# Optimization experiments

Measured on AMD Instinct MI355X. Metric: run time of the kernel, lower is better.

Reference implementation:

```python
import jax, jax.numpy as jnp
import numpy as np

N_RNA, N_PROT = 50000, 20000
S, E = 4, 500000
D_IN = 1024


def setup_inputs() -> dict:
    key = jax.random.key(0)
    ks = jax.random.split(key, 12)
    return {
        "rna_rows": jax.random.randint(ks[0], (S, E), 0, N_RNA, dtype=jnp.int32),
        "rna_cols": jax.random.randint(ks[1], (S, E), 0, N_PROT, dtype=jnp.int32),
        "rna_vals": jax.random.uniform(ks[2], (S, E), dtype=jnp.float32),
        "prot_rows": jax.random.randint(ks[3], (S, E), 0, N_PROT, dtype=jnp.int32),
        "prot_cols": jax.random.randint(ks[4], (S, E), 0, N_RNA, dtype=jnp.int32),
        "prot_vals": jax.random.uniform(ks[5], (S, E), dtype=jnp.float32),
        "H_rna": jax.random.normal(ks[6], (N_RNA, D_IN), dtype=jnp.float32),
        "H_prot": jax.random.normal(ks[7], (N_PROT, D_IN), dtype=jnp.float32),
        "w0": jax.random.normal(ks[8], (S, 1024, 128), dtype=jnp.float32) * 0.04,
        "sw0": jax.random.normal(ks[9], (1024, 512), dtype=jnp.float32) * 0.04,
        "w1": jax.random.normal(ks[10], (S, 512, 64), dtype=jnp.float32) * 0.06,
        "sw1": jax.random.normal(ks[11], (512, 256), dtype=jnp.float32) * 0.06,
    }


def _spmm_all(rows, cols, vals, x, n_out):
    # rows/cols/vals: [S, E]; x: [S, n_in, k] -> [S, n_out, k]
    def one(r, c, v, xs):
        return jax.ops.segment_sum(v[:, None] * xs[c], r, num_segments=n_out)
    return jax.vmap(one)(rows, cols, vals, x)


def reference(rna_rows, rna_cols, rna_vals, prot_rows, prot_cols, prot_vals,
              H_rna, H_prot, w0, sw0, w1, sw1):
    n_rna, n_prot = H_rna.shape[0], H_prot.shape[0]
    for W, SW in ((w0, sw0), (w1, sw1)):
        s, _, k = W.shape
        # per-relation dense transform: [S, n, k]
        tmp_u = jnp.einsum('nd,sdk->snk', H_rna, W)
        tmp_v = jnp.einsum('nd,sdk->snk', H_prot, W)
        # sparse aggregation across the bipartite graph
        rna_h = _spmm_all(rna_rows, rna_cols, rna_vals, tmp_v, n_rna)     # [S, n_rna, k]
        prot_h = _spmm_all(prot_rows, prot_cols, prot_vals, tmp_u, n_prot)
        # concat over relations (matches torch.cat along dim=1)
        rna_h = jnp.transpose(rna_h, (1, 0, 2)).reshape(n_rna, s * k)
        prot_h = jnp.transpose(prot_h, (1, 0, 2)).reshape(n_prot, s * k)
        # self-loop residual; dropout=0.0 (eval) is identity; relu activation
        H_rna = jax.nn.relu(rna_h + H_rna @ SW)
        H_prot = jax.nn.relu(prot_h + H_prot @ SW)
    return H_rna, H_prot
```

## Files before the change

kernel.cpp:

```cpp
#include <hip/hip_runtime.h>
#include <hip/hip_bf16.h>


typedef unsigned short u16;
typedef short s16x8 __attribute__((ext_vector_type(8)));
typedef float f32x4 __attribute__((ext_vector_type(4)));
typedef __attribute__((ext_vector_type(8))) unsigned short u16x8;
typedef __attribute__((ext_vector_type(2))) unsigned short u16x2;
typedef unsigned long long u64;

__device__ __forceinline__ u16 f2bf(float x) {
    unsigned u = __float_as_uint(x);
    return (u16)((u + 0x7fff + ((u >> 16) & 1)) >> 16);
}
__device__ __forceinline__ float bf2f(u16 h) {
    return __uint_as_float(((unsigned)h) << 16);
}

__device__ __forceinline__ void gload16(const u16* g, u16* l) {
    __builtin_amdgcn_global_load_lds(
        (const __attribute__((address_space(1))) unsigned int*)g,
        (__attribute__((address_space(3))) unsigned int*)l,
        16, 0, 0);
}

__global__ __launch_bounds__(256)
void gemm_bf16_kernel(const u16* __restrict__ Ah, const u16* __restrict__ Bh,
                      u16* __restrict__ Y, int ldy,
                      int K, int nxmask, int nxshift)
{
    __shared__ u16 lds[2][2][4096];

    const int nwg = gridDim.x;
    const int q   = nwg >> 3, r8 = nwg & 7;
    const int xcd = blockIdx.x & 7, pos = blockIdx.x >> 3;
    const int lin = (xcd < r8 ? xcd * (q + 1) : r8 * (q + 1) + (xcd - r8) * q) + pos;
    const int bm0 = (lin >> nxshift) * 128;
    const int bn0 = (lin & nxmask) * 128;

    const int tid  = threadIdx.x;
    const int lane = tid & 63;
    const int wid  = tid >> 6;
    const int wr   = wid >> 1;
    const int wc   = wid & 1;

    const int srow = tid >> 2;
    const int scol = ((tid & 3) ^ ((tid >> 3) & 3)) * 8;
    const size_t aoff0 = (size_t)(bm0 + srow) * K + scol;
    const size_t aoff1 = (size_t)(bm0 + srow + 64) * K + scol;
    const size_t boff0 = (size_t)(bn0 + srow) * K + scol;
    const size_t boff1 = (size_t)(bn0 + srow + 64) * K + scol;
    const int c0 = tid * 8;
    const int c1 = 2048 + tid * 8;

    u16* L0 = &lds[0][0][0];

    f32x4 zero = {0.f, 0.f, 0.f, 0.f};
    f32x4 acc[4][4];
    #pragma unroll
    for (int i = 0; i < 4; ++i)
        #pragma unroll
        for (int j = 0; j < 4; ++j) acc[i][j] = zero;

    const int fchunk = (((lane >> 4) ^ ((lane >> 1) & 3))) * 8;
    const int a_fr = (wr * 64 + (lane & 15)) * 32 + fchunk;
    const int b_fr = (wc * 64 + (lane & 15)) * 32 + fchunk;

    const int nk = K >> 5;

    {
        u16* L = L0;
        gload16(Ah + aoff0, L + c0);          gload16(Ah + aoff1, L + c1);
        gload16(Bh + boff0, L + 4096 + c0);   gload16(Bh + boff1, L + 4096 + c1);
    }
    int cur = 0;
    for (int t = 0; t < nk; ++t) {
        if (t + 1 < nk) {
            const int k0 = (t + 1) * 32;
            u16* L = L0 + (cur ^ 1) * 8192;
            gload16(Ah + aoff0 + k0, L + c0);         gload16(Ah + aoff1 + k0, L + c1);
            gload16(Bh + boff0 + k0, L + 4096 + c0);  gload16(Bh + boff1 + k0, L + 4096 + c1);
            asm volatile("s_waitcnt vmcnt(4)\n\ts_barrier" ::: "memory");
        } else {
            asm volatile("s_waitcnt vmcnt(0)\n\ts_barrier" ::: "memory");
        }
        const u16* L = L0 + cur * 8192;
        s16x8 bh[4];
        #pragma unroll
        for (int nf = 0; nf < 4; ++nf)
            bh[nf] = *(const s16x8*)(L + 4096 + b_fr + nf * 512);
        #pragma unroll
        for (int mf = 0; mf < 4; ++mf) {
            s16x8 ahv = *(const s16x8*)(L + a_fr + mf * 512);
            #pragma unroll
            for (int nf = 0; nf < 4; ++nf)
                acc[mf][nf] = __builtin_amdgcn_mfma_f32_16x16x32_bf16(ahv, bh[nf], acc[mf][nf], 0, 0, 0);
        }
        asm volatile("s_barrier" ::: "memory");
        cur ^= 1;
    }

    #pragma unroll
    for (int mf = 0; mf < 4; ++mf) {
        const int row0 = bm0 + wr * 64 + mf * 16 + (lane >> 4) * 4;
        #pragma unroll
        for (int nf = 0; nf < 4; ++nf) {
            const int col = bn0 + wc * 64 + nf * 16 + (lane & 15);
            #pragma unroll
            for (int r = 0; r < 4; ++r)
                Y[(size_t)(row0 + r) * ldy + col] = f2bf(acc[mf][nf][r]);
        }
    }
}

__global__ __launch_bounds__(256)
void cvt_bf16_kernel(const float* __restrict__ A, u16* __restrict__ Hh,
                     int M, int kshift)
{
    const size_t g  = (size_t)blockIdx.x * 256 + threadIdx.x;
    const size_t i8 = g * 8;
    const int row   = (int)(i8 >> kshift);
    f32x4 a = {0.f, 0.f, 0.f, 0.f}, b = {0.f, 0.f, 0.f, 0.f};
    if (row < M) {
        a = *(const f32x4*)(A + i8);
        b = *(const f32x4*)(A + i8 + 4);
    }
    u16x8 h;
    #pragma unroll
    for (int j = 0; j < 4; ++j) { h[j] = f2bf(a[j]); h[4 + j] = f2bf(b[j]); }
    *(u16x8*)(Hh + i8) = h;
}

__global__ __launch_bounds__(256)
void zero_u16_kernel(u16* __restrict__ a, int n)
{
    int i = blockIdx.x * 256 + threadIdx.x;
    if (i < n) a[i] = 0;
}

__global__ __launch_bounds__(256)
void zero2_i32_kernel(int* __restrict__ a, int na, int* __restrict__ b, int nb)
{
    int i = blockIdx.x * 256 + threadIdx.x;
    if (i < na) a[i] = 0;
    if (i < nb) b[i] = 0;
}

__global__ __launch_bounds__(256)
void pack_rows2_kernel(const int* __restrict__ rowsR, const int* __restrict__ rowsP,
                       u16* __restrict__ r16R, u16* __restrict__ r16P, int E)
{
    int s = blockIdx.y;
    int e = (blockIdx.x * 256 + threadIdx.x) * 4;
    if (e >= E) return;
    const int* rows = blockIdx.z ? rowsP : rowsR;
    u16* r16 = blockIdx.z ? r16P : r16R;
    size_t base = (size_t)s * E;
    if (e + 4 <= E) {
        int4 r4 = *(const int4*)(rows + base + e);
        u16 p[4] = {(u16)r4.x, (u16)r4.y, (u16)r4.z, (u16)r4.w};
        *(u64*)(r16 + base + e) = *(const u64*)p;
    } else {
        for (int j = 0; j < 4 && e + j < E; ++j)
            r16[base + e + j] = (u16)rows[base + e + j];
    }
}

__global__ __launch_bounds__(256)
void hist2_kernel(const u16* __restrict__ rowsR, const u16* __restrict__ rowsP,
                  int* __restrict__ cntR, int* __restrict__ cntP,
                  int NR, int NP, int E)
{
    int s = blockIdx.y;
    int e = blockIdx.x * 256 + threadIdx.x;
    if (e >= E) return;
    if (blockIdx.z == 0) atomicAdd(cntR + s * NR + (int)rowsR[(size_t)s * E + e], 1);
    else                 atomicAdd(cntP + s * NP + (int)rowsP[(size_t)s * E + e], 1);
}

__global__ __launch_bounds__(256)
void scan_block2_kernel(const int* __restrict__ cR, int* __restrict__ rpR,
                        int* __restrict__ bsR, int NR, int np1R, int NBR,
                        const int* __restrict__ cP, int* __restrict__ rpP,
                        int* __restrict__ bsP, int NP, int np1P, int NBP)
{
    const int side = blockIdx.z;
    const int NB = side ? NBP : NBR;
    if ((int)blockIdx.x >= NB) return;
    const int N = side ? NP : NR;
    const int np1 = side ? np1P : np1R;
    const int* counts = side ? cP : cR;
    int* rowptr = side ? rpP : rpR;
    int* blocksum = side ? bsP : bsR;

    __shared__ int sd[256];
    int s = blockIdx.y;
    int i = blockIdx.x * 256 + threadIdx.x;
    int tid = threadIdx.x;
    int v = (i < N) ? counts[s * N + i] : 0;
    sd[tid] = v;
    __syncthreads();
    #pragma unroll
    for (int off = 1; off < 256; off <<= 1) {
        int t = (tid >= off) ? sd[tid - off] : 0;
        __syncthreads();
        sd[tid] += t;
        __syncthreads();
    }
    if (i < N) rowptr[s * np1 + i] = sd[tid] - v;
    if (tid == 255) blocksum[s * NB + blockIdx.x] = sd[255];
}

__global__ __launch_bounds__(256)
void scan_aux2_kernel(int* __restrict__ bsR, int NBR, int* __restrict__ bsP, int NBP)
{
    const int side = blockIdx.x >> 2;
    const int s = blockIdx.x & 3;
    int* blocksum = side ? bsP : bsR;
    const int NB = side ? NBP : NBR;

    __shared__ int sd[256];
    int tid = threadIdx.x;
    int v = (tid < NB) ? blocksum[s * NB + tid] : 0;
    sd[tid] = v;
    __syncthreads();
    #pragma unroll
    for (int off = 1; off < 256; off <<= 1) {
        int t = (tid >= off) ? sd[tid - off] : 0;
        __syncthreads();
        sd[tid] += t;
        __syncthreads();
    }
    if (tid < NB) blocksum[s * NB + tid] = sd[tid] - v;
}

__global__ __launch_bounds__(256)
void finalize2_kernel(int* __restrict__ rpR, const int* __restrict__ bsR,
                      int* __restrict__ curR, int NR, int np1R, int NBR,
                      int* __restrict__ rpP, const int* __restrict__ bsP,
                      int* __restrict__ curP, int NP, int np1P, int NBP, int E)
{
    const int side = blockIdx.z;
    const int NB = side ? NBP : NBR;
    if ((int)blockIdx.x >= NB) return;
    const int N = side ? NP : NR;
    const int np1 = side ? np1P : np1R;
    int* rowptr = side ? rpP : rpR;
    const int* blocksum = side ? bsP : bsR;
    int* cursor = side ? curP : curR;

    int s = blockIdx.y;
    int i = blockIdx.x * 256 + threadIdx.x;
    if (i < N) {
        int v = rowptr[s * np1 + i] + blocksum[s * NB + blockIdx.x];
        rowptr[s * np1 + i] = v;
        cursor[s * N + i] = v;
    }
    if (i == N) rowptr[s * np1 + N] = E;
}

__global__ __launch_bounds__(256)
void fill_sliced_kernel(const u16* __restrict__ r16R, const int* __restrict__ colsR,
                        const float* __restrict__ valsR,
                        const u16* __restrict__ r16P, const int* __restrict__ colsP,
                        const float* __restrict__ valsP,
                        int* __restrict__ curR, int* __restrict__ curP,
                        int2* __restrict__ evR, int2* __restrict__ evP,
                        int NR, int NP, int E)
{
    const int slice = blockIdx.x & 7;
    const int chunk = blockIdx.x >> 3;
    const int s     = blockIdx.y;
    const int side  = blockIdx.z;
    const int N          = side ? NP : NR;
    const u16* r16       = side ? r16P : r16R;
    const int* cols      = side ? colsP : colsR;
    const float* vals    = side ? valsP : valsR;
    int* cursor          = side ? curP : curR;
    int2* ev             = side ? evP : evR;

    const int Nsl = (N + 7) >> 3;
    const int r0 = slice * Nsl;
    const int r1 = min(N, r0 + Nsl);

    const int e0 = chunk * 1024 + threadIdx.x * 4;
    if (e0 >= E) return;
    const size_t base = (size_t)s * E;

    if (e0 + 4 <= E) {
        u64 rq = __builtin_nontemporal_load((const u64*)(r16 + base + e0));
        int rr[4] = {(int)(u16)rq, (int)(u16)(rq >> 16),
                     (int)(u16)(rq >> 32), (int)(u16)(rq >> 48)};
        #pragma unroll
        for (int j = 0; j < 4; ++j) {
            if (rr[j] >= r0 && rr[j] < r1) {
                int   c = __builtin_nontemporal_load(cols + base + e0 + j);
                float v = __builtin_nontemporal_load(vals + base + e0 + j);
                int pos = atomicAdd(cursor + s * N + rr[j], 1);
                ev[base + pos] = make_int2(c, __float_as_int(v));
            }
        }
    } else {
        for (int j = 0; j < 4 && e0 + j < E; ++j) {
            int r = (int)r16[base + e0 + j];
            if (r >= r0 && r < r1) {
                int pos = atomicAdd(cursor + s * N + r, 1);
                ev[base + pos] = make_int2(cols[base + e0 + j],
                                           __float_as_int(vals[base + e0 + j]));
            }
        }
    }
}

template<int KCH, int MODE>
__global__ __launch_bounds__(256)
void spmm2_kernel(const int* __restrict__ rpR, const int* __restrict__ rpP,
                  int np1R, int np1P,
                  const int2* __restrict__ evRg, const int2* __restrict__ evPg,
                  const u16* __restrict__ InR, const u16* __restrict__ InP, int ldi,
                  u16* __restrict__ BaseR, u16* __restrict__ BaseP, int ldb,
                  u16* __restrict__ OHR, u16* __restrict__ OHP,
                  float* __restrict__ OFR, float* __restrict__ OFP, int ldo,
                  int NR, int E)
{
    int r = blockIdx.x;
    const int s    = threadIdx.x >> 6;
    const int lane = threadIdx.x & 63;
    const int* rp; const int2* ev; const u16* In; u16* Base; int np1;
    u16* OH; float* OF;
    if (r < NR) { rp = rpR; ev = evRg; In = InR; Base = BaseR; np1 = np1R;
                  OH = OHR; OF = OFR; }
    else { r -= NR; rp = rpP; ev = evPg; In = InP; Base = BaseP; np1 = np1P;
           OH = OHP; OF = OFP; }
    int e0 = __builtin_amdgcn_readfirstlane(rp[s * np1 + r]);
    int e1 = __builtin_amdgcn_readfirstlane(rp[s * np1 + r + 1]);
    if (MODE == 0 && e0 == e1) return;
    ev += (size_t)s * E;

    if (KCH == 128) {
        const int qg = lane >> 4;
        const int ql = lane & 15;
        const int col = s * 128 + ql * 8;
        float a[8] = {0.f, 0.f, 0.f, 0.f, 0.f, 0.f, 0.f, 0.f};
        int e = e0;
        for (; e + 7 < e1; e += 8) {
            int2 p0 = ev[e + qg];
            int2 p1 = ev[e + 4 + qg];
            float v0 = __int_as_float(p0.y);
            float v1 = __int_as_float(p1.y);
            u16x8 x0 = *(const u16x8*)(In + (size_t)p0.x * ldi + col);
            u16x8 x1 = *(const u16x8*)(In + (size_t)p1.x * ldi + col);
            #pragma unroll
            for (int j = 0; j < 8; ++j)
                a[j] += v0 * bf2f(x0[j]) + v1 * bf2f(x1[j]);
        }
        for (; e < e1; e += 4) {
            if (e + qg < e1) {
                int2 pv = ev[e + qg];
                float v = __int_as_float(pv.y);
                u16x8 x = *(const u16x8*)(In + (size_t)pv.x * ldi + col);
                #pragma unroll
                for (int j = 0; j < 8; ++j)
                    a[j] += v * bf2f(x[j]);
            }
        }
        #pragma unroll
        for (int j = 0; j < 8; ++j) {
            a[j] += __shfl_xor(a[j], 16);
            a[j] += __shfl_xor(a[j], 32);
        }
        if (lane < 16) {
            u16x8* bp = (u16x8*)(Base + (size_t)r * ldb + col);
            u16x8 b = *bp;
            if (MODE == 0) {
                u16x8 nb;
                #pragma unroll
                for (int j = 0; j < 8; ++j) nb[j] = f2bf(bf2f(b[j]) + a[j]);
                *bp = nb;
            } else if (MODE == 1) {
                u16x8 h;
                #pragma unroll
                for (int j = 0; j < 8; ++j) h[j] = f2bf(fmaxf(bf2f(b[j]) + a[j], 0.f));
                *(u16x8*)(OH + (size_t)r * ldo + col) = h;
            } else {
                f32x4 o0, o1;
                #pragma unroll
                for (int j = 0; j < 4; ++j) {
                    o0[j] = fmaxf(bf2f(b[j]) + a[j], 0.f);
                    o1[j] = fmaxf(bf2f(b[4 + j]) + a[4 + j], 0.f);
                }
                *(f32x4*)(OF + (size_t)r * ldo + col) = o0;
                *(f32x4*)(OF + (size_t)r * ldo + col + 4) = o1;
            }
        }
    } else {
        const int og = lane >> 3;
        const int ol = lane & 7;
        const int col = s * 64 + ol * 8;
        float a[8] = {0.f, 0.f, 0.f, 0.f, 0.f, 0.f, 0.f, 0.f};
        int e = e0;
        for (; e + 15 < e1; e += 16) {
            int2 p0 = ev[e + og];
            int2 p1 = ev[e + 8 + og];
            float v0 = __int_as_float(p0.y);
            float v1 = __int_as_float(p1.y);
            u16x8 x0 = *(const u16x8*)(In + (size_t)p0.x * ldi + col);
            u16x8 x1 = *(const u16x8*)(In + (size_t)p1.x * ldi + col);
            #pragma unroll
            for (int j = 0; j < 8; ++j)
                a[j] += v0 * bf2f(x0[j]) + v1 * bf2f(x1[j]);
        }
        for (; e < e1; e += 8) {
            if (e + og < e1) {
                int2 pv = ev[e + og];
                float v = __int_as_float(pv.y);
                u16x8 x = *(const u16x8*)(In + (size_t)pv.x * ldi + col);
                #pragma unroll
                for (int j = 0; j < 8; ++j)
                    a[j] += v * bf2f(x[j]);
            }
        }
        #pragma unroll
        for (int j = 0; j < 8; ++j) {
            a[j] += __shfl_xor(a[j], 8);
            a[j] += __shfl_xor(a[j], 16);
            a[j] += __shfl_xor(a[j], 32);
        }
        if (lane < 8) {
            u16x8* bp = (u16x8*)(Base + (size_t)r * ldb + col);
            u16x8 b = *bp;
            if (MODE == 0) {
                u16x8 nb;
                #pragma unroll
                for (int j = 0; j < 8; ++j) nb[j] = f2bf(bf2f(b[j]) + a[j]);
                *bp = nb;
            } else {
                f32x4 o0, o1;
                #pragma unroll
                for (int j = 0; j < 4; ++j) {
                    o0[j] = fmaxf(bf2f(b[j]) + a[j], 0.f);
                    o1[j] = fmaxf(bf2f(b[4 + j]) + a[4 + j], 0.f);
                }
                *(f32x4*)(OF + (size_t)r * ldo + col) = o0;
                *(f32x4*)(OF + (size_t)r * ldo + col + 4) = o1;
            }
        }
    }
}

__global__ __launch_bounds__(256)
void relu_out_kernel(const u16* __restrict__ Z, int ld, int coff,
                     float* __restrict__ out, int M)
{
    int g = blockIdx.x * 256 + threadIdx.x;
    if (g >= M * 256) return;
    int row = g >> 8;
    int col = g & 255;
    out[g] = fmaxf(bf2f(Z[(size_t)row * ld + coff + col]), 0.f);
}

__global__ __launch_bounds__(256)
void pack_b0_kernel(const float* __restrict__ w0, const float* __restrict__ sw0,
                    u16* __restrict__ Bh)
{
    int g = blockIdx.x * 256 + threadIdx.x;
    int j = g >> 10, d = g & 1023;
    float v;
    if (j < 512) v = w0[((size_t)(j >> 7) * 1024 + d) * 128 + (j & 127)];
    else         v = sw0[(size_t)d * 512 + (j - 512)];
    Bh[g] = f2bf(v);
}

__global__ __launch_bounds__(256)
void pack_b1_kernel(const float* __restrict__ w1, const float* __restrict__ sw1,
                    u16* __restrict__ Bh)
{
    int g = blockIdx.x * 256 + threadIdx.x;
    int j = g >> 9, d = g & 511;
    float v;
    if (j < 256) v = w1[((size_t)(j >> 6) * 512 + d) * 64 + (j & 63)];
    else         v = sw1[(size_t)d * 256 + (j - 256)];
    Bh[g] = f2bf(v);
}

extern "C" void kernel_launch(void* const* d_in, const int* in_sizes, int n_in,
                              void* d_out, int out_size, void* d_ws, size_t ws_size,
                              hipStream_t stream)
{
    const int*   rna_rows  = (const int*)  d_in[0];
    const int*   rna_cols  = (const int*)  d_in[1];
    const float* rna_vals  = (const float*)d_in[2];
    const int*   prot_rows = (const int*)  d_in[3];
    const int*   prot_cols = (const int*)  d_in[4];
    const float* prot_vals = (const float*)d_in[5];
    const float* H_rna     = (const float*)d_in[6];
    const float* H_prot    = (const float*)d_in[7];
    const float* w0        = (const float*)d_in[8];
    const float* sw0       = (const float*)d_in[9];
    const float* w1        = (const float*)d_in[10];
    const float* sw1       = (const float*)d_in[11];

    const int NRNA = 50000, NPROT = 20000, S = 4, E = 500000;
    const int MP_RNA = 50048, MP_PROT = 20096;
    const int MP_ALL = MP_RNA + MP_PROT;
    const int NP1_R = NRNA + 1, NP1_P = NPROT + 1;
    const int NB_R = (NRNA + 255) / 256;
    const int NB_P = (NPROT + 255) / 256;
    const int EB   = (E + 255) / 256;
    const int EB4  = (E + 1023) / 1024;

    char* ws = (char*)d_ws;
    size_t off = 0;
    u16*   Y16   = (u16*)  (ws + off); off += (size_t)MP_ALL * 1024 * 2;
    u16*   Ahbig = (u16*)  (ws + off); off += (size_t)MP_ALL * 1024 * 2;
    u16*   B0h   = (u16*)  (ws + off); off += (size_t)1024 * 1024 * 2;
    u16*   B1h   = (u16*)  (ws + off); off += (size_t)512 * 512 * 2;
    size_t base_bytes = off;

    u16* AhR = Ahbig;
    u16* AhP = Ahbig + (size_t)MP_RNA * 512;

    size_t csr_bytes = 0;
    csr_bytes += (size_t)S * E * 8 * 2;
    csr_bytes += (size_t)S * E * 2 * 2;
    csr_bytes += ((size_t)S * (NRNA * 2 + NP1_R + NB_R)) * 4;
    csr_bytes += ((size_t)S * (NPROT * 2 + NP1_P + NB_P)) * 4;
    const bool csr_in_ws = (ws_size >= base_bytes + csr_bytes);

    char* csr = csr_in_ws ? (ws + base_bytes) : (char*)d_out;
    size_t coff = 0;
    int2*  evR     = (int2*) (csr + coff); coff += (size_t)S * E * 8;
    int2*  evP     = (int2*) (csr + coff); coff += (size_t)S * E * 8;
    u16*   r16R    = (u16*)  (csr + coff); coff += (size_t)S * E * 2;
    u16*   r16P    = (u16*)  (csr + coff); coff += (size_t)S * E * 2;
    int*   countsR = (int*)  (csr + coff); coff += (size_t)S * NRNA * 4;
    int*   rowptrR = (int*)  (csr + coff); coff += (size_t)S * NP1_R * 4;
    int*   cursorR = (int*)  (csr + coff); coff += (size_t)S * NRNA * 4;
    int*   bsumR   = (int*)  (csr + coff); coff += (size_t)S * NB_R * 4;
    int*   countsP = (int*)  (csr + coff); coff += (size_t)S * NPROT * 4;
    int*   rowptrP = (int*)  (csr + coff); coff += (size_t)S * NP1_P * 4;
    int*   cursorP = (int*)  (csr + coff); coff += (size_t)S * NPROT * 4;
    int*   bsumP   = (int*)  (csr + coff); coff += (size_t)S * NB_P * 4;

    dim3 blk(256);
    float* out = (float*)d_out;

    pack_b0_kernel<<<(1024 * 1024) / 256, blk, 0, stream>>>(w0, sw0, B0h);
    pack_b1_kernel<<<(512 * 512) / 256, blk, 0, stream>>>(w1, sw1, B1h);

    pack_rows2_kernel<<<dim3(EB4, S, 2), blk, 0, stream>>>(rna_rows, prot_rows,
                                                           r16R, r16P, E);
    zero2_i32_kernel<<<(S * NRNA + 255) / 256, blk, 0, stream>>>(countsR, S * NRNA,
                                                                 countsP, S * NPROT);
    hist2_kernel<<<dim3(EB, S, 2), blk, 0, stream>>>(r16R, r16P,
                                                     countsR, countsP, NRNA, NPROT, E);
    scan_block2_kernel<<<dim3(NB_R, S, 2), blk, 0, stream>>>(
        countsR, rowptrR, bsumR, NRNA, NP1_R, NB_R,
        countsP, rowptrP, bsumP, NPROT, NP1_P, NB_P);
    scan_aux2_kernel<<<8, blk, 0, stream>>>(bsumR, NB_R, bsumP, NB_P);
    finalize2_kernel<<<dim3(NB_R, S, 2), blk, 0, stream>>>(
        rowptrR, bsumR, cursorR, NRNA, NP1_R, NB_R,
        rowptrP, bsumP, cursorP, NPROT, NP1_P, NB_P, E);
    fill_sliced_kernel<<<dim3(EB4 * 8, S, 2), blk, 0, stream>>>(
        r16R, rna_cols, rna_vals, r16P, prot_cols, prot_vals,
        cursorR, cursorP, evR, evP, NRNA, NPROT, E);

    cvt_bf16_kernel<<<MP_RNA / 2, blk, 0, stream>>>(H_rna, Ahbig, NRNA, 10);
    cvt_bf16_kernel<<<MP_PROT / 2, blk, 0, stream>>>(H_prot, Ahbig + (size_t)MP_RNA * 1024,
                                                     NPROT, 10);
    gemm_bf16_kernel<<<8 * (MP_ALL / 128), blk, 0, stream>>>(
        Ahbig, B0h, Y16, 1024, 1024, 7, 3);

    spmm2_kernel<128, 1><<<NRNA + NPROT, blk, 0, stream>>>(
        rowptrR, rowptrP, NP1_R, NP1_P, evR, evP,
        Y16 + (size_t)MP_RNA * 1024,
        Y16,
        1024,
        Y16 + 512, Y16 + (size_t)MP_RNA * 1024 + 512, 1024,
        AhR, AhP, nullptr, nullptr, 512,
        NRNA, E);

    zero_u16_kernel<<<(48 * 512 + 255) / 256, blk, 0, stream>>>(
        AhR + (size_t)NRNA * 512, 48 * 512);
    zero_u16_kernel<<<(96 * 512 + 255) / 256, blk, 0, stream>>>(
        AhP + (size_t)NPROT * 512, 96 * 512);

    gemm_bf16_kernel<<<4 * (MP_ALL / 128), blk, 0, stream>>>(
        Ahbig, B1h, Y16, 512, 512, 3, 2);

    if (csr_in_ws) {
        spmm2_kernel<64, 2><<<NRNA + NPROT, blk, 0, stream>>>(
            rowptrR, rowptrP, NP1_R, NP1_P, evR, evP,
            Y16 + (size_t)MP_RNA * 512, Y16, 512,
            Y16 + 256, Y16 + (size_t)MP_RNA * 512 + 256, 512,
            nullptr, nullptr,
            out, out + (size_t)NRNA * 256, 256,
            NRNA, E);
    } else {
        spmm2_kernel<64, 0><<<NRNA + NPROT, blk, 0, stream>>>(
            rowptrR, rowptrP, NP1_R, NP1_P, evR, evP,
            Y16 + (size_t)MP_RNA * 512, Y16, 512,
            Y16 + 256, Y16 + (size_t)MP_RNA * 512 + 256, 512,
            nullptr, nullptr,
            nullptr, nullptr, 0,
            NRNA, E);
        relu_out_kernel<<<(NRNA * 256) / 256, blk, 0, stream>>>(Y16, 512, 256, out, NRNA);
        relu_out_kernel<<<(NPROT * 256) / 256, blk, 0, stream>>>(
            Y16 + (size_t)MP_RNA * 512, 512, 256, out + (size_t)NRNA * 256, NPROT);
    }
}
```

Baseline: 990.3 us.

## Fuse CSR fill into first GEMM launch to overlap scatter with matmul

```diff
diff --git a/kernel.cpp b/kernel.cpp
--- a/kernel.cpp
+++ b/kernel.cpp
@@ -6,7 +6,6 @@
 typedef short s16x8 __attribute__((ext_vector_type(8)));
 typedef float f32x4 __attribute__((ext_vector_type(4)));
 typedef __attribute__((ext_vector_type(8))) unsigned short u16x8;
-typedef __attribute__((ext_vector_type(2))) unsigned short u16x2;
 typedef unsigned long long u64;
 
 __device__ __forceinline__ u16 f2bf(float x) {
@@ -24,16 +23,13 @@
         16, 0, 0);
 }
 
-__global__ __launch_bounds__(256)
-void gemm_bf16_kernel(const u16* __restrict__ Ah, const u16* __restrict__ Bh,
-                      u16* __restrict__ Y, int ldy,
-                      int K, int nxmask, int nxshift)
-{
-    __shared__ u16 lds[2][2][4096];
-
-    const int nwg = gridDim.x;
+__device__ __forceinline__
+void gemm_body(u16* ldsb, int bx, int nwg,
+               const u16* __restrict__ Ah, const u16* __restrict__ Bh,
+               u16* __restrict__ Y, int ldy, int K, int nxmask, int nxshift)
+{
     const int q   = nwg >> 3, r8 = nwg & 7;
-    const int xcd = blockIdx.x & 7, pos = blockIdx.x >> 3;
+    const int xcd = bx & 7, pos = bx >> 3;
     const int lin = (xcd < r8 ? xcd * (q + 1) : r8 * (q + 1) + (xcd - r8) * q) + pos;
     const int bm0 = (lin >> nxshift) * 128;
     const int bn0 = (lin & nxmask) * 128;
@@ -53,8 +49,6 @@
     const int c0 = tid * 8;
     const int c1 = 2048 + tid * 8;
 
-    u16* L0 = &lds[0][0][0];
-
     f32x4 zero = {0.f, 0.f, 0.f, 0.f};
     f32x4 acc[4][4];
     #pragma unroll
@@ -69,7 +63,7 @@
     const int nk = K >> 5;
 
     {
-        u16* L = L0;
+        u16* L = ldsb;
         gload16(Ah + aoff0, L + c0);          gload16(Ah + aoff1, L + c1);
         gload16(Bh + boff0, L + 4096 + c0);   gload16(Bh + boff1, L + 4096 + c1);
     }
@@ -77,14 +71,14 @@
     for (int t = 0; t < nk; ++t) {
         if (t + 1 < nk) {
             const int k0 = (t + 1) * 32;
-            u16* L = L0 + (cur ^ 1) * 8192;
+            u16* L = ldsb + (cur ^ 1) * 8192;
             gload16(Ah + aoff0 + k0, L + c0);         gload16(Ah + aoff1 + k0, L + c1);
             gload16(Bh + boff0 + k0, L + 4096 + c0);  gload16(Bh + boff1 + k0, L + 4096 + c1);
             asm volatile("s_waitcnt vmcnt(4)\n\ts_barrier" ::: "memory");
         } else {
             asm volatile("s_waitcnt vmcnt(0)\n\ts_barrier" ::: "memory");
         }
-        const u16* L = L0 + cur * 8192;
+        const u16* L = ldsb + cur * 8192;
         s16x8 bh[4];
         #pragma unroll
         for (int nf = 0; nf < 4; ++nf)
@@ -110,6 +104,90 @@
             for (int r = 0; r < 4; ++r)
                 Y[(size_t)(row0 + r) * ldy + col] = f2bf(acc[mf][nf][r]);
         }
+    }
+}
+
+__global__ __launch_bounds__(256)
+void gemm_bf16_kernel(const u16* __restrict__ Ah, const u16* __restrict__ Bh,
+                      u16* __restrict__ Y, int ldy,
+                      int K, int nxmask, int nxshift)
+{
+    __shared__ u16 lds[2][2][4096];
+    gemm_body(&lds[0][0][0], blockIdx.x, gridDim.x, Ah, Bh, Y, ldy, K, nxmask, nxshift);
+}
+
+__device__ __forceinline__
+void fill_body(int fx, int s, int side,
+               const u16* __restrict__ r16R, const int* __restrict__ colsR,
+               const float* __restrict__ valsR,
+               const u16* __restrict__ r16P, const int* __restrict__ colsP,
+               const float* __restrict__ valsP,
+               int* __restrict__ curR, int* __restrict__ curP,
+               int2* __restrict__ evR, int2* __restrict__ evP,
+               int NR, int NP, int E)
+{
+    const int slice = fx & 7;
+    const int chunk = fx >> 3;
+    const int N          = side ? NP : NR;
+    const u16* r16       = side ? r16P : r16R;
+    const int* cols      = side ? colsP : colsR;
+    const float* vals    = side ? valsP : valsR;
+    int* cursor          = side ? curP : curR;
+    int2* ev             = side ? evP : evR;
+
+    const int Nsl = (N + 7) >> 3;
+    const int r0 = slice * Nsl;
+    const int r1 = min(N, r0 + Nsl);
+
+    const int e0 = chunk * 1024 + threadIdx.x * 4;
+    if (e0 >= E) return;
+    const size_t base = (size_t)s * E;
+
+    if (e0 + 4 <= E) {
+        u64 rq = *(const u64*)(r16 + base + e0);
+        int rr[4] = {(int)(u16)rq, (int)(u16)(rq >> 16),
+                     (int)(u16)(rq >> 32), (int)(u16)(rq >> 48)};
+        #pragma unroll
+        for (int j = 0; j < 4; ++j) {
+            if (rr[j] >= r0 && rr[j] < r1) {
+                int pos = atomicAdd(cursor + s * N + rr[j], 1);
+                ev[base + pos] = make_int2(cols[base + e0 + j],
+                                           __float_as_int(vals[base + e0 + j]));
+            }
+        }
+    } else {
+        for (int j = 0; j < 4 && e0 + j < E; ++j) {
+            int r = (int)r16[base + e0 + j];
+            if (r >= r0 && r < r1) {
+                int pos = atomicAdd(cursor + s * N + r, 1);
+                ev[base + pos] = make_int2(cols[base + e0 + j],
+                                           __float_as_int(vals[base + e0 + j]));
+            }
+        }
+    }
+}
+
+__global__ __launch_bounds__(256)
+void fused_gemm_fill_kernel(const u16* __restrict__ Ah, const u16* __restrict__ Bh,
+                            u16* __restrict__ Y, int ldy, int K,
+                            int nxmask, int nxshift, int GG,
+                            const u16* __restrict__ r16R, const int* __restrict__ colsR,
+                            const float* __restrict__ valsR,
+                            const u16* __restrict__ r16P, const int* __restrict__ colsP,
+                            const float* __restrict__ valsP,
+                            int* __restrict__ curR, int* __restrict__ curP,
+                            int2* __restrict__ evR, int2* __restrict__ evP,
+                            int NR, int NP, int E)
+{
+    __shared__ u16 lds[2][2][4096];
+    const int bx = blockIdx.x;
+    if (bx < GG) {
+        if (blockIdx.y || blockIdx.z) return;
+        gemm_body(&lds[0][0][0], bx, GG, Ah, Bh, Y, ldy, K, nxmask, nxshift);
+    } else {
+        fill_body(bx - GG, blockIdx.y, blockIdx.z,
+                  r16R, colsR, valsR, r16P, colsP, valsP,
+                  curR, curP, evR, evP, NR, NP, E);
     }
 }
 
@@ -257,59 +335,6 @@
         cursor[s * N + i] = v;
     }
     if (i == N) rowptr[s * np1 + N] = E;
-}
-
-__global__ __launch_bounds__(256)
-void fill_sliced_kernel(const u16* __restrict__ r16R, const int* __restrict__ colsR,
-                        const float* __restrict__ valsR,
-                        const u16* __restrict__ r16P, const int* __restrict__ colsP,
-                        const float* __restrict__ valsP,
-                        int* __restrict__ curR, int* __restrict__ curP,
-                        int2* __restrict__ evR, int2* __restrict__ evP,
-                        int NR, int NP, int E)
-{
-    const int slice = blockIdx.x & 7;
-    const int chunk = blockIdx.x >> 3;
-    const int s     = blockIdx.y;
-    const int side  = blockIdx.z;
-    const int N          = side ? NP : NR;
-    const u16* r16       = side ? r16P : r16R;
-    const int* cols      = side ? colsP : colsR;
-    const float* vals    = side ? valsP : valsR;
-    int* cursor          = side ? curP : curR;
-    int2* ev             = side ? evP : evR;
-
-    const int Nsl = (N + 7) >> 3;
-    const int r0 = slice * Nsl;
-    const int r1 = min(N, r0 + Nsl);
-
-    const int e0 = chunk * 1024 + threadIdx.x * 4;
-    if (e0 >= E) return;
-    const size_t base = (size_t)s * E;
-
-    if (e0 + 4 <= E) {
-        u64 rq = __builtin_nontemporal_load((const u64*)(r16 + base + e0));
-        int rr[4] = {(int)(u16)rq, (int)(u16)(rq >> 16),
-                     (int)(u16)(rq >> 32), (int)(u16)(rq >> 48)};
-        #pragma unroll
-        for (int j = 0; j < 4; ++j) {
-            if (rr[j] >= r0 && rr[j] < r1) {
-                int   c = __builtin_nontemporal_load(cols + base + e0 + j);
-                float v = __builtin_nontemporal_load(vals + base + e0 + j);
-                int pos = atomicAdd(cursor + s * N + rr[j], 1);
-                ev[base + pos] = make_int2(c, __float_as_int(v));
-            }
-        }
-    } else {
-        for (int j = 0; j < 4 && e0 + j < E; ++j) {
-            int r = (int)r16[base + e0 + j];
-            if (r >= r0 && r < r1) {
-                int pos = atomicAdd(cursor + s * N + r, 1);
-                ev[base + pos] = make_int2(cols[base + e0 + j],
-                                           __float_as_int(vals[base + e0 + j]));
-            }
-        }
-    }
 }
 
 template<int KCH, int MODE>
@@ -508,6 +533,8 @@
     const int NB_P = (NPROT + 255) / 256;
     const int EB   = (E + 255) / 256;
     const int EB4  = (E + 1023) / 1024;
+    const int GG   = 8 * (MP_ALL / 128);
+    const int FX   = EB4 * 8;
 
     char* ws = (char*)d_ws;
     size_t off = 0;
@@ -561,15 +588,15 @@
     finalize2_kernel<<<dim3(NB_R, S, 2), blk, 0, stream>>>(
         rowptrR, bsumR, cursorR, NRNA, NP1_R, NB_R,
         rowptrP, bsumP, cursorP, NPROT, NP1_P, NB_P, E);
-    fill_sliced_kernel<<<dim3(EB4 * 8, S, 2), blk, 0, stream>>>(
-        r16R, rna_cols, rna_vals, r16P, prot_cols, prot_vals,
-        cursorR, cursorP, evR, evP, NRNA, NPROT, E);
 
     cvt_bf16_kernel<<<MP_RNA / 2, blk, 0, stream>>>(H_rna, Ahbig, NRNA, 10);
     cvt_bf16_kernel<<<MP_PROT / 2, blk, 0, stream>>>(H_prot, Ahbig + (size_t)MP_RNA * 1024,
                                                      NPROT, 10);
-    gemm_bf16_kernel<<<8 * (MP_ALL / 128), blk, 0, stream>>>(
-        Ahbig, B0h, Y16, 1024, 1024, 7, 3);
+
+    fused_gemm_fill_kernel<<<dim3(GG + FX, S, 2), blk, 0, stream>>>(
+        Ahbig, B0h, Y16, 1024, 1024, 7, 3, GG,
+        r16R, rna_cols, rna_vals, r16P, prot_cols, prot_vals,
+        cursorR, cursorP, evR, evP, NRNA, NPROT, E);
 
     spmm2_kernel<128, 1><<<NRNA + NPROT, blk, 0, stream>>>(
         rowptrR, rowptrP, NP1_R, NP1_P, evR, evP,
```

Result: no change. 981.7 us (-0.9%).

## Fuse row packing with histogram and merge bf16 conversion with CSR fill

Applied to the files above, without the earlier changes.

```diff
diff --git a/kernel.cpp b/kernel.cpp
--- a/kernel.cpp
+++ b/kernel.cpp
@@ -6,7 +6,6 @@
 typedef short s16x8 __attribute__((ext_vector_type(8)));
 typedef float f32x4 __attribute__((ext_vector_type(4)));
 typedef __attribute__((ext_vector_type(8))) unsigned short u16x8;
-typedef __attribute__((ext_vector_type(2))) unsigned short u16x2;
 typedef unsigned long long u64;
 
 __device__ __forceinline__ u16 f2bf(float x) {
@@ -113,13 +112,12 @@
     }
 }
 
-__global__ __launch_bounds__(256)
-void cvt_bf16_kernel(const float* __restrict__ A, u16* __restrict__ Hh,
-                     int M, int kshift)
-{
-    const size_t g  = (size_t)blockIdx.x * 256 + threadIdx.x;
+__device__ __forceinline__
+void cvt_body(int bid, const float* __restrict__ A, u16* __restrict__ Hh, int M)
+{
+    const size_t g  = (size_t)bid * 256 + threadIdx.x;
     const size_t i8 = g * 8;
-    const int row   = (int)(i8 >> kshift);
+    const int row   = (int)(i8 >> 10);
     f32x4 a = {0.f, 0.f, 0.f, 0.f}, b = {0.f, 0.f, 0.f, 0.f};
     if (row < M) {
         a = *(const f32x4*)(A + i8);
@@ -131,6 +129,89 @@
     *(u16x8*)(Hh + i8) = h;
 }
 
+__device__ __forceinline__
+void fill_body16(int fx, int s, int side,
+                 const u16* __restrict__ r16R, const int* __restrict__ colsR,
+                 const float* __restrict__ valsR,
+                 const u16* __restrict__ r16P, const int* __restrict__ colsP,
+                 const float* __restrict__ valsP,
+                 int* __restrict__ curR, int* __restrict__ curP,
+                 int2* __restrict__ evR, int2* __restrict__ evP,
+                 int NR, int NP, int E)
+{
+    const int slice = fx & 7;
+    const int chunk = fx >> 3;
+    const int N          = side ? NP : NR;
+    const u16* r16       = side ? r16P : r16R;
+    const int* cols      = side ? colsP : colsR;
+    const float* vals    = side ? valsP : valsR;
+    int* cursor          = side ? curP : curR;
+    int2* ev             = side ? evP : evR;
+
+    const int Nsl = (N + 7) >> 3;
+    const int r0 = slice * Nsl;
+    const int r1 = min(N, r0 + Nsl);
+
+    const int e0 = chunk * 4096 + threadIdx.x * 16;
+    if (e0 >= E) return;
+    const size_t base = (size_t)s * E;
+
+    if (e0 + 16 <= E) {
+        u64 rq[4];
+        #pragma unroll
+        for (int g = 0; g < 4; ++g)
+            rq[g] = *(const u64*)(r16 + base + e0 + g * 4);
+        #pragma unroll
+        for (int g = 0; g < 4; ++g) {
+            #pragma unroll
+            for (int j = 0; j < 4; ++j) {
+                int r = (int)(u16)(rq[g] >> (16 * j));
+                if (r >= r0 && r < r1) {
+                    int idx = e0 + g * 4 + j;
+                    int pos = atomicAdd(cursor + s * N + r, 1);
+                    ev[base + pos] = make_int2(cols[base + idx],
+                                               __float_as_int(vals[base + idx]));
+                }
+            }
+        }
+    } else {
+        for (int j = 0; j < 16 && e0 + j < E; ++j) {
+            int r = (int)r16[base + e0 + j];
+            if (r >= r0 && r < r1) {
+                int pos = atomicAdd(cursor + s * N + r, 1);
+                ev[base + pos] = make_int2(cols[base + e0 + j],
+                                           __float_as_int(vals[base + e0 + j]));
+            }
+        }
+    }
+}
+
+__global__ __launch_bounds__(256)
+void fused_cvt_fill_kernel(const float* __restrict__ H_rna, const float* __restrict__ H_prot,
+                           u16* __restrict__ AhR_full, u16* __restrict__ AhP_full,
+                           int CVR, int CV, int XW,
+                           const u16* __restrict__ r16R, const int* __restrict__ colsR,
+                           const float* __restrict__ valsR,
+                           const u16* __restrict__ r16P, const int* __restrict__ colsP,
+                           const float* __restrict__ valsP,
+                           int* __restrict__ curR, int* __restrict__ curP,
+                           int2* __restrict__ evR, int2* __restrict__ evP,
+                           int NR, int NP, int E, int FX16)
+{
+    const int z = blockIdx.z;
+    if (z == 0) {
+        int id = blockIdx.y * XW + blockIdx.x;
+        if (id >= CV) return;
+        if (id < CVR) cvt_body(id, H_rna, AhR_full, NR);
+        else          cvt_body(id - CVR, H_prot, AhP_full, NP);
+    } else {
+        if ((int)blockIdx.x >= FX16) return;
+        fill_body16(blockIdx.x, blockIdx.y, z - 1,
+                    r16R, colsR, valsR, r16P, colsP, valsP,
+                    curR, curP, evR, evP, NR, NP, E);
+    }
+}
+
 __global__ __launch_bounds__(256)
 void zero_u16_kernel(u16* __restrict__ a, int n)
 {
@@ -147,35 +228,34 @@
 }
 
 __global__ __launch_bounds__(256)
-void pack_rows2_kernel(const int* __restrict__ rowsR, const int* __restrict__ rowsP,
-                       u16* __restrict__ r16R, u16* __restrict__ r16P, int E)
+void pack_hist2_kernel(const int* __restrict__ rowsR, const int* __restrict__ rowsP,
+                       u16* __restrict__ r16R, u16* __restrict__ r16P,
+                       int* __restrict__ cntR, int* __restrict__ cntP,
+                       int NR, int NP, int E)
 {
     int s = blockIdx.y;
     int e = (blockIdx.x * 256 + threadIdx.x) * 4;
     if (e >= E) return;
     const int* rows = blockIdx.z ? rowsP : rowsR;
     u16* r16 = blockIdx.z ? r16P : r16R;
+    int* cnt = blockIdx.z ? cntP : cntR;
+    const int N = blockIdx.z ? NP : NR;
     size_t base = (size_t)s * E;
     if (e + 4 <= E) {
         int4 r4 = *(const int4*)(rows + base + e);
         u16 p[4] = {(u16)r4.x, (u16)r4.y, (u16)r4.z, (u16)r4.w};
         *(u64*)(r16 + base + e) = *(const u64*)p;
+        atomicAdd(cnt + s * N + r4.x, 1);
+        atomicAdd(cnt + s * N + r4.y, 1);
+        atomicAdd(cnt + s * N + r4.z, 1);
+        atomicAdd(cnt + s * N + r4.w, 1);
     } else {
-        for (int j = 0; j < 4 && e + j < E; ++j)
-            r16[base + e + j] = (u16)rows[base + e + j];
-    }
-}
-
-__global__ __launch_bounds__(256)
-void hist2_kernel(const u16* __restrict__ rowsR, const u16* __restrict__ rowsP,
-                  int* __restrict__ cntR, int* __restrict__ cntP,
-                  int NR, int NP, int E)
-{
-    int s = blockIdx.y;
-    int e = blockIdx.x * 256 + threadIdx.x;
-    if (e >= E) return;
-    if (blockIdx.z == 0) atomicAdd(cntR + s * NR + (int)rowsR[(size_t)s * E + e], 1);
-    else                 atomicAdd(cntP + s * NP + (int)rowsP[(size_t)s * E + e], 1);
+        for (int j = 0; j < 4 && e + j < E; ++j) {
+            int r = rows[base + e + j];
+            r16[base + e + j] = (u16)r;
+            atomicAdd(cnt + s * N + r, 1);
+        }
+    }
 }
 
 __global__ __launch_bounds__(256)
@@ -257,59 +337,6 @@
         cursor[s * N + i] = v;
     }
     if (i == N) rowptr[s * np1 + N] = E;
-}
-
-__global__ __launch_bounds__(256)
-void fill_sliced_kernel(const u16* __restrict__ r16R, const int* __restrict__ colsR,
-                        const float* __restrict__ valsR,
-                        const u16* __restrict__ r16P, const int* __restrict__ colsP,
-                        const float* __restrict__ valsP,
-                        int* __restrict__ curR, int* __restrict__ curP,
-                        int2* __restrict__ evR, int2* __restrict__ evP,
-                        int NR, int NP, int E)
-{
-    const int slice = blockIdx.x & 7;
-    const int chunk = blockIdx.x >> 3;
-    const int s     = blockIdx.y;
-    const int side  = blockIdx.z;
-    const int N          = side ? NP : NR;
-    const u16* r16       = side ? r16P : r16R;
-    const int* cols      = side ? colsP : colsR;
-    const float* vals    = side ? valsP : valsR;
-    int* cursor          = side ? curP : curR;
-    int2* ev             = side ? evP : evR;
-
-    const int Nsl = (N + 7) >> 3;
-    const int r0 = slice * Nsl;
-    const int r1 = min(N, r0 + Nsl);
-
-    const int e0 = chunk * 1024 + threadIdx.x * 4;
-    if (e0 >= E) return;
-    const size_t base = (size_t)s * E;
-
-    if (e0 + 4 <= E) {
-        u64 rq = __builtin_nontemporal_load((const u64*)(r16 + base + e0));
-        int rr[4] = {(int)(u16)rq, (int)(u16)(rq >> 16),
-                     (int)(u16)(rq >> 32), (int)(u16)(rq >> 48)};
-        #pragma unroll
-        for (int j = 0; j < 4; ++j) {
-            if (rr[j] >= r0 && rr[j] < r1) {
-                int   c = __builtin_nontemporal_load(cols + base + e0 + j);
-                float v = __builtin_nontemporal_load(vals + base + e0 + j);
-                int pos = atomicAdd(cursor + s * N + rr[j], 1);
-                ev[base + pos] = make_int2(c, __float_as_int(v));
-            }
-        }
-    } else {
-        for (int j = 0; j < 4 && e0 + j < E; ++j) {
-            int r = (int)r16[base + e0 + j];
-            if (r >= r0 && r < r1) {
-                int pos = atomicAdd(cursor + s * N + r, 1);
-                ev[base + pos] = make_int2(cols[base + e0 + j],
-                                           __float_as_int(vals[base + e0 + j]));
-            }
-        }
-    }
 }
 
 template<int KCH, int MODE>
@@ -506,8 +533,12 @@
     const int NP1_R = NRNA + 1, NP1_P = NPROT + 1;
     const int NB_R = (NRNA + 255) / 256;
     const int NB_P = (NPROT + 255) / 256;
-    const int EB   = (E + 255) / 256;
     const int EB4  = (E + 1023) / 1024;
+    const int EB16 = (E + 4095) / 4096;
+    const int FX16 = EB16 * 8;
+    const int CVR  = MP_RNA / 2, CVP = MP_PROT / 2;
+    const int CV   = CVR + CVP;
+    const int XW   = (CV + 3) / 4;
 
     char* ws = (char*)d_ws;
     size_t off = 0;
@@ -548,12 +579,10 @@
     pack_b0_kernel<<<(1024 * 1024) / 256, blk, 0, stream>>>(w0, sw0, B0h);
     pack_b1_kernel<<<(512 * 512) / 256, blk, 0, stream>>>(w1, sw1, B1h);
 
-    pack_rows2_kernel<<<dim3(EB4, S, 2), blk, 0, stream>>>(rna_rows, prot_rows,
-                                                           r16R, r16P, E);
     zero2_i32_kernel<<<(S * NRNA + 255) / 256, blk, 0, stream>>>(countsR, S * NRNA,
                                                                  countsP, S * NPROT);
-    hist2_kernel<<<dim3(EB, S, 2), blk, 0, stream>>>(r16R, r16P,
-                                                     countsR, countsP, NRNA, NPROT, E);
+    pack_hist2_kernel<<<dim3(EB4, S, 2), blk, 0, stream>>>(
+        rna_rows, prot_rows, r16R, r16P, countsR, countsP, NRNA, NPROT, E);
     scan_block2_kernel<<<dim3(NB_R, S, 2), blk, 0, stream>>>(
         countsR, rowptrR, bsumR, NRNA, NP1_R, NB_R,
         countsP, rowptrP, bsumP, NPROT, NP1_P, NB_P);
@@ -561,13 +590,12 @@
     finalize2_kernel<<<dim3(NB_R, S, 2), blk, 0, stream>>>(
         rowptrR, bsumR, cursorR, NRNA, NP1_R, NB_R,
         rowptrP, bsumP, cursorP, NPROT, NP1_P, NB_P, E);
-    fill_sliced_kernel<<<dim3(EB4 * 8, S, 2), blk, 0, stream>>>(
+
+    fused_cvt_fill_kernel<<<dim3(XW, 4, 3), blk, 0, stream>>>(
+        H_rna, H_prot, Ahbig, Ahbig + (size_t)MP_RNA * 1024, CVR, CV, XW,
         r16R, rna_cols, rna_vals, r16P, prot_cols, prot_vals,
-        cursorR, cursorP, evR, evP, NRNA, NPROT, E);
-
-    cvt_bf16_kernel<<<MP_RNA / 2, blk, 0, stream>>>(H_rna, Ahbig, NRNA, 10);
-    cvt_bf16_kernel<<<MP_PROT / 2, blk, 0, stream>>>(H_prot, Ahbig + (size_t)MP_RNA * 1024,
-                                                     NPROT, 10);
+        cursorR, cursorP, evR, evP, NRNA, NPROT, E, FX16);
+
     gemm_bf16_kernel<<<8 * (MP_ALL / 128), blk, 0, stream>>>(
         Ahbig, B0h, Y16, 1024, 1024, 7, 3);
 
```

Result: faster. 962.9 us (median of 2 runs) (-2.8%).
